# Performance work log

Measured on AMD Instinct MI355X. Metric: run time of the kernel, lower is better.

## Reference

```python
import jax, jax.numpy as jnp
import numpy as np

EPS = 1e-12  # torch F.normalize eps

def _l2norm(x, axis):
    n = jnp.sqrt(jnp.sum(x * x, axis=axis, keepdims=True))
    return x / jnp.maximum(n, EPS)

def setup_inputs() -> dict:
    key = jax.random.key(0)
    k1, k2, k3, k4 = jax.random.split(key, 4)
    B, Lq, Ld, D, NWAY = 128, 32, 180, 128, 8
    query_reps = jax.random.normal(k1, (B, Lq, D), dtype=jnp.float32)
    doc_reps = jax.random.normal(k2, (B, NWAY, Ld, D), dtype=jnp.float32)
    doc_mask = jax.random.randint(k3, (B, NWAY, Ld), 0, 2, dtype=jnp.int32)
    # labels are teacher log-probabilities (KLDivLoss log_target=True)
    labels = jax.nn.log_softmax(jax.random.normal(k4, (B, NWAY), dtype=jnp.float32), axis=-1)
    return {"query_reps": query_reps, "doc_reps": doc_reps, "doc_mask": doc_mask, "labels": labels}

def reference(query_reps, doc_reps, doc_mask, labels):
    # query: L2-normalize over feature dim (dim=2 in torch call)
    q = _l2norm(query_reps, axis=-1)                      # [B, Lq, D]
    # docs: mask padding tokens, then F.normalize with DEFAULT dim=1,
    # i.e. L2-normalize along the token axis (faithful to source).
    d = doc_reps * doc_mask[..., None].astype(doc_reps.dtype)  # [B, W, Ld, D]
    d = _l2norm(d, axis=2)
    # MaxSim: sim[b,w,q,l] = <q_bq, d_bwl>; max over doc tokens, sum over query tokens
    sim = jnp.einsum('bqd,bwld->bwql', q, d)              # [B, W, Lq, Ld]
    scores = jnp.max(sim, axis=-1).sum(axis=-1)           # [B, W]
    log_p = jax.nn.log_softmax(scores, axis=-1)           # == log(softmax(scores))
    # KLDivLoss(log_target=True, reduction='batchmean'): sum(exp(t)*(t - x)) / B
    B = scores.shape[0]
    loss = jnp.sum(jnp.exp(labels) * (labels - log_p)) / B
    return loss  # torch.mean of a scalar is the scalar
```

## Files before the change

kernel.cpp:

```cpp
#include <hip/hip_runtime.h>
#include <math.h>
#include <stdint.h>

#define NB 128
#define LQ 32
#define LD 180
#define DD 128
#define NW 8
#define NBW (NB*NW)
#define PB 40
#define LROWS 192

typedef __attribute__((ext_vector_type(8)))  short short8v;
typedef __attribute__((ext_vector_type(16))) float f32x16;

static __device__ __forceinline__ short bf16_rne(float f) {
    uint32_t u = __float_as_uint(f);
    uint32_t r = (u + 0x7fffu + ((u >> 16) & 1u)) >> 16;
    return (short)r;
}
static __device__ __forceinline__ float bf16_f32(short h) {
    return __uint_as_float(((uint32_t)(uint16_t)h) << 16);
}

__global__ __launch_bounds__(256) void qnorm_kernel(
    const float* __restrict__ qreps, float* __restrict__ qinv)
{
    const int t = threadIdx.x, b = blockIdx.x;
    const int r = t >> 3, sub = t & 7;
    const float4* qr = (const float4*)(qreps + (size_t)b * LQ * DD + r * DD + sub * 16);
    float ss = 0.f;
    #pragma unroll
    for (int k = 0; k < 4; ++k) {
        float4 v = qr[k];
        ss += v.x * v.x + v.y * v.y + v.z * v.z + v.w * v.w;
    }
    ss += __shfl_xor(ss, 4);
    ss += __shfl_xor(ss, 2);
    ss += __shfl_xor(ss, 1);
    if (sub == 0) qinv[b * LQ + r] = 1.0f / fmaxf(sqrtf(ss), 1e-12f);
}

__global__ __launch_bounds__(256, 4) void maxsim_kernel(
    const float* __restrict__ qreps, const float* __restrict__ dreps,
    const int* __restrict__ dmask, const float* __restrict__ qinv,
    float* __restrict__ scores)
{
    __shared__ short s_dh[LROWS * PB];
    __shared__ short s_dl[LROWS * PB];
    __shared__ short s_qh[LQ * PB];
    __shared__ short s_ql[LQ * PB];
    __shared__ float s_ssq[32 * 32];
    __shared__ float s_dinv[32];
    __shared__ float s_pm[4][LQ];

    const int t = threadIdx.x, bw = blockIdx.x, b = bw >> 3;
    const int lane = t & 63, wave = t >> 6;
    const int d4 = t & 7;
    const int rbase = t >> 3;
    const int lh = lane >> 5;
    const int l31 = lane & 31;

    const float4* doc4  = (const float4*)(dreps + (size_t)bw * LD * DD);
    const float4* q4g   = (const float4*)(qreps + (size_t)b * LQ * DD);
    const float*  qinvb = qinv + b * LQ;
    const int*    mrow  = dmask + bw * LD;

    float mk[6];
    #pragma unroll
    for (int s = 0; s < 6; ++s) {
        int l = rbase + 32 * s;
        mk[s] = (l < LD) ? (float)mrow[l] : 0.0f;
    }

    f32x16 acc0 = {};
    f32x16 acc1 = {};

    for (int cc = 0; cc < 4; ++cc) {
        if (cc) __syncthreads();

        float4 qv = q4g[rbase * 32 + cc * 8 + d4];

        float4 pssq = make_float4(0.f, 0.f, 0.f, 0.f);
        #pragma unroll
        for (int s = 0; s < 6; ++s) {
            int l = rbase + 32 * s;
            if (l < LD) {
                float4 v = doc4[l * 32 + cc * 8 + d4];
                float m = mk[s];
                v.x *= m; v.y *= m; v.z *= m; v.w *= m;
                pssq.x += v.x * v.x; pssq.y += v.y * v.y;
                pssq.z += v.z * v.z; pssq.w += v.w * v.w;
                short4 h, lo;
                h.x = bf16_rne(v.x); h.y = bf16_rne(v.y);
                h.z = bf16_rne(v.z); h.w = bf16_rne(v.w);
                lo.x = bf16_rne(v.x - bf16_f32(h.x));
                lo.y = bf16_rne(v.y - bf16_f32(h.y));
                lo.z = bf16_rne(v.z - bf16_f32(h.z));
                lo.w = bf16_rne(v.w - bf16_f32(h.w));
                *(short4*)&s_dh[l * PB + 4 * d4] = h;
                *(short4*)&s_dl[l * PB + 4 * d4] = lo;
            } else {
                short4 z = make_short4(0, 0, 0, 0);
                *(short4*)&s_dh[l * PB + 4 * d4] = z;
                *(short4*)&s_dl[l * PB + 4 * d4] = z;
            }
        }
        *(float4*)&s_ssq[rbase * 32 + 4 * d4] = pssq;
        __syncthreads();

        if (t < 32) {
            float tot = 0.f;
            #pragma unroll
            for (int g = 0; g < 32; ++g) tot += s_ssq[g * 32 + t];
            s_dinv[t] = 1.0f / fmaxf(sqrtf(tot), 1e-12f);
        }
        __syncthreads();

        {
            float qi = qinvb[rbase];
            float4 di = *(const float4*)&s_dinv[4 * d4];
            qv.x *= qi * di.x; qv.y *= qi * di.y;
            qv.z *= qi * di.z; qv.w *= qi * di.w;
            short4 h, lo;
            h.x = bf16_rne(qv.x); h.y = bf16_rne(qv.y);
            h.z = bf16_rne(qv.z); h.w = bf16_rne(qv.w);
            lo.x = bf16_rne(qv.x - bf16_f32(h.x));
            lo.y = bf16_rne(qv.y - bf16_f32(h.y));
            lo.z = bf16_rne(qv.z - bf16_f32(h.z));
            lo.w = bf16_rne(qv.w - bf16_f32(h.w));
            *(short4*)&s_qh[rbase * PB + 4 * d4] = h;
            *(short4*)&s_ql[rbase * PB + 4 * d4] = lo;
        }
        __syncthreads();

        #pragma unroll
        for (int kk = 0; kk < 2; ++kk) {
            const int ao = l31 * PB + 16 * kk + 8 * lh;
            short8v ah = *(const short8v*)&s_qh[ao];
            short8v al = *(const short8v*)&s_ql[ao];
            const int bo0 = (32 * wave + l31) * PB + 16 * kk + 8 * lh;
            short8v bh = *(const short8v*)&s_dh[bo0];
            short8v bl = *(const short8v*)&s_dl[bo0];
            acc0 = __builtin_amdgcn_mfma_f32_32x32x16_bf16(ah, bh, acc0, 0, 0, 0);
            acc0 = __builtin_amdgcn_mfma_f32_32x32x16_bf16(ah, bl, acc0, 0, 0, 0);
            acc0 = __builtin_amdgcn_mfma_f32_32x32x16_bf16(al, bh, acc0, 0, 0, 0);
            if (wave < 2) {
                const int bo1 = (32 * (wave + 4) + l31) * PB + 16 * kk + 8 * lh;
                short8v bh1 = *(const short8v*)&s_dh[bo1];
                short8v bl1 = *(const short8v*)&s_dl[bo1];
                acc1 = __builtin_amdgcn_mfma_f32_32x32x16_bf16(ah, bh1, acc1, 0, 0, 0);
                acc1 = __builtin_amdgcn_mfma_f32_32x32x16_bf16(ah, bl1, acc1, 0, 0, 0);
                acc1 = __builtin_amdgcn_mfma_f32_32x32x16_bf16(al, bh1, acc1, 0, 0, 0);
            }
        }
    }

    float pm[16];
    #pragma unroll
    for (int r = 0; r < 16; ++r) {
        float v = acc0[r];
        if (wave < 2) v = fmaxf(v, acc1[r]);
        pm[r] = v;
    }
    #pragma unroll
    for (int off = 1; off <= 16; off <<= 1)
        #pragma unroll
        for (int r = 0; r < 16; ++r)
            pm[r] = fmaxf(pm[r], __shfl_xor(pm[r], off));
    if (l31 == 0) {
        #pragma unroll
        for (int r = 0; r < 16; ++r)
            s_pm[wave][(r & 3) + 8 * (r >> 2) + 4 * lh] = pm[r];
    }
    __syncthreads();
    if (t < LQ) {
        float v = fmaxf(fmaxf(s_pm[0][t], s_pm[1][t]),
                        fmaxf(s_pm[2][t], s_pm[3][t]));
        #pragma unroll
        for (int off = 16; off >= 1; off >>= 1) v += __shfl_xor(v, off);
        if (t == 0) scores[bw] = v;
    }
}

__global__ __launch_bounds__(NB) void finish_kernel(
    const float* __restrict__ scores, const float* __restrict__ labels,
    float* __restrict__ out)
{
    __shared__ float s_part[2];
    const int t = threadIdx.x;
    const float* sr = scores + t * NW;
    const float* lr = labels + t * NW;

    float s[NW];
    float m = -INFINITY;
    #pragma unroll
    for (int w = 0; w < NW; ++w) { s[w] = sr[w]; m = fmaxf(m, s[w]); }
    float se = 0.f;
    #pragma unroll
    for (int w = 0; w < NW; ++w) se += expf(s[w] - m);
    float lse = logf(se) + m;

    float term = 0.f;
    #pragma unroll
    for (int w = 0; w < NW; ++w) {
        float lw = lr[w];
        term += expf(lw) * (lw - (s[w] - lse));
    }
    #pragma unroll
    for (int off = 32; off > 0; off >>= 1) term += __shfl_xor(term, off);
    if ((t & 63) == 0) s_part[t >> 6] = term;
    __syncthreads();
    if (t == 0) out[0] = (s_part[0] + s_part[1]) / (float)NB;
}

extern "C" void kernel_launch(void* const* d_in, const int* in_sizes, int n_in,
                              void* d_out, int out_size, void* d_ws, size_t ws_size,
                              hipStream_t stream) {
    const float* qreps  = (const float*)d_in[0];
    const float* dreps  = (const float*)d_in[1];
    const int*   dmask  = (const int*)d_in[2];
    const float* labels = (const float*)d_in[3];
    float* out = (float*)d_out;

    float* scores = (float*)d_ws;
    float* qinv   = scores + NBW;

    qnorm_kernel<<<NB, 256, 0, stream>>>(qreps, qinv);
    maxsim_kernel<<<NBW, 256, 0, stream>>>(qreps, dreps, dmask, qinv, scores);
    finish_kernel<<<1, NB, 0, stream>>>(scores, labels, out);
}
```

Before: 156.9 us.

## Fuse query norm into maxsim, use 512 threads, prefetch next doc chunk

Removes the separate query-normalisation kernel by computing query inverse norms inside each maxsim block. Blocks grow to 512 threads, so six waves each own one 32-row doc tile instead of four waves with two of them doing double work. The next K-chunk of doc and query data is register-prefetched while the current chunk is converted. Also cheaper bf16 splitting (truncation instead of RNE), a shuffle-based partial sum-of-squares reduction, and lighter barriers. The cost is redundant query-norm work per block, higher register pressure, and two idle waves during the MFMA phase.

```diff
diff --git a/kernel.cpp b/kernel.cpp
--- a/kernel.cpp
+++ b/kernel.cpp
@@ -14,169 +14,183 @@
 typedef __attribute__((ext_vector_type(8)))  short short8v;
 typedef __attribute__((ext_vector_type(16))) float f32x16;
 
-static __device__ __forceinline__ short bf16_rne(float f) {
-    uint32_t u = __float_as_uint(f);
-    uint32_t r = (u + 0x7fffu + ((u >> 16) & 1u)) >> 16;
-    return (short)r;
-}
-static __device__ __forceinline__ float bf16_f32(short h) {
-    return __uint_as_float(((uint32_t)(uint16_t)h) << 16);
-}
-
-__global__ __launch_bounds__(256) void qnorm_kernel(
-    const float* __restrict__ qreps, float* __restrict__ qinv)
-{
-    const int t = threadIdx.x, b = blockIdx.x;
-    const int r = t >> 3, sub = t & 7;
-    const float4* qr = (const float4*)(qreps + (size_t)b * LQ * DD + r * DD + sub * 16);
-    float ss = 0.f;
-    #pragma unroll
-    for (int k = 0; k < 4; ++k) {
-        float4 v = qr[k];
-        ss += v.x * v.x + v.y * v.y + v.z * v.z + v.w * v.w;
-    }
-    ss += __shfl_xor(ss, 4);
-    ss += __shfl_xor(ss, 2);
-    ss += __shfl_xor(ss, 1);
-    if (sub == 0) qinv[b * LQ + r] = 1.0f / fmaxf(sqrtf(ss), 1e-12f);
-}
-
-__global__ __launch_bounds__(256, 4) void maxsim_kernel(
+static __device__ __forceinline__ void bar() {
+    asm volatile("s_waitcnt lgkmcnt(0)" ::: "memory");
+    __builtin_amdgcn_s_barrier();
+}
+
+static __device__ __forceinline__ void split2(float x, short& h, short& l) {
+    uint32_t u = __float_as_uint(x);
+    h = (short)(u >> 16);
+    float r = x - __uint_as_float(u & 0xffff0000u);
+    l = (short)(__float_as_uint(r) >> 16);
+}
+
+__global__ __launch_bounds__(512, 4) void maxsim_kernel(
     const float* __restrict__ qreps, const float* __restrict__ dreps,
-    const int* __restrict__ dmask, const float* __restrict__ qinv,
-    float* __restrict__ scores)
+    const int* __restrict__ dmask, float* __restrict__ scores)
 {
     __shared__ short s_dh[LROWS * PB];
     __shared__ short s_dl[LROWS * PB];
     __shared__ short s_qh[LQ * PB];
     __shared__ short s_ql[LQ * PB];
-    __shared__ float s_ssq[32 * 32];
+    __shared__ float s_ssq[8 * 32];
     __shared__ float s_dinv[32];
-    __shared__ float s_pm[4][LQ];
+    __shared__ float s_qinv[32];
+    __shared__ float s_pm[6][LQ];
 
     const int t = threadIdx.x, bw = blockIdx.x, b = bw >> 3;
     const int lane = t & 63, wave = t >> 6;
     const int d4 = t & 7;
-    const int rbase = t >> 3;
-    const int lh = lane >> 5;
-    const int l31 = lane & 31;
-
-    const float4* doc4  = (const float4*)(dreps + (size_t)bw * LD * DD);
-    const float4* q4g   = (const float4*)(qreps + (size_t)b * LQ * DD);
-    const float*  qinvb = qinv + b * LQ;
-    const int*    mrow  = dmask + bw * LD;
-
-    float mk[6];
-    #pragma unroll
-    for (int s = 0; s < 6; ++s) {
-        int l = rbase + 32 * s;
-        mk[s] = (l < LD) ? (float)mrow[l] : 0.0f;
-    }
-
-    f32x16 acc0 = {};
-    f32x16 acc1 = {};
-
+    const int rb = t >> 3;
+    const int lh = lane >> 5, l31 = lane & 31;
+
+    const float4* doc4 = (const float4*)(dreps + (size_t)bw * LD * DD);
+    const float4* q4g  = (const float4*)(qreps + (size_t)b * LQ * DD);
+    const int*    mrow = dmask + bw * LD;
+
+    float4 dv0 = doc4[(rb      ) * 32 + d4];
+    float4 dv1 = doc4[(rb + 64 ) * 32 + d4];
+    float4 dv2;
+    if (rb < 52) dv2 = doc4[(rb + 128) * 32 + d4];
+    float4 qv, qn;
+    if (t < 256) qv = q4g[(t >> 3) * 32 + d4];
+
+    const float mk0 = (float)mrow[rb];
+    const float mk1 = (float)mrow[rb + 64];
+    const float mk2 = (rb < 52) ? (float)mrow[rb + 128] : 0.0f;
+
+    {
+        int r = t >> 4, sub = t & 15;
+        float4 a = q4g[r * 32 + sub];
+        float4 c = q4g[r * 32 + 16 + sub];
+        float ss = a.x*a.x + a.y*a.y + a.z*a.z + a.w*a.w
+                 + c.x*c.x + c.y*c.y + c.z*c.z + c.w*c.w;
+        ss += __shfl_xor(ss, 8);
+        ss += __shfl_xor(ss, 4);
+        ss += __shfl_xor(ss, 2);
+        ss += __shfl_xor(ss, 1);
+        if (sub == 0) s_qinv[r] = 1.0f / fmaxf(sqrtf(ss), 1e-12f);
+    }
+
+    f32x16 acc = {};
+
+    #pragma unroll
     for (int cc = 0; cc < 4; ++cc) {
-        if (cc) __syncthreads();
-
-        float4 qv = q4g[rbase * 32 + cc * 8 + d4];
+        if (cc) bar();
 
         float4 pssq = make_float4(0.f, 0.f, 0.f, 0.f);
-        #pragma unroll
-        for (int s = 0; s < 6; ++s) {
-            int l = rbase + 32 * s;
-            if (l < LD) {
-                float4 v = doc4[l * 32 + cc * 8 + d4];
-                float m = mk[s];
-                v.x *= m; v.y *= m; v.z *= m; v.w *= m;
-                pssq.x += v.x * v.x; pssq.y += v.y * v.y;
-                pssq.z += v.z * v.z; pssq.w += v.w * v.w;
-                short4 h, lo;
-                h.x = bf16_rne(v.x); h.y = bf16_rne(v.y);
-                h.z = bf16_rne(v.z); h.w = bf16_rne(v.w);
-                lo.x = bf16_rne(v.x - bf16_f32(h.x));
-                lo.y = bf16_rne(v.y - bf16_f32(h.y));
-                lo.z = bf16_rne(v.z - bf16_f32(h.z));
-                lo.w = bf16_rne(v.w - bf16_f32(h.w));
-                *(short4*)&s_dh[l * PB + 4 * d4] = h;
-                *(short4*)&s_dl[l * PB + 4 * d4] = lo;
-            } else {
-                short4 z = make_short4(0, 0, 0, 0);
-                *(short4*)&s_dh[l * PB + 4 * d4] = z;
-                *(short4*)&s_dl[l * PB + 4 * d4] = z;
-            }
-        }
-        *(float4*)&s_ssq[rbase * 32 + 4 * d4] = pssq;
-        __syncthreads();
+        {
+            float4 v = dv0; float m = mk0;
+            v.x *= m; v.y *= m; v.z *= m; v.w *= m;
+            pssq.x += v.x*v.x; pssq.y += v.y*v.y; pssq.z += v.z*v.z; pssq.w += v.w*v.w;
+            short4 h, lo;
+            split2(v.x, h.x, lo.x); split2(v.y, h.y, lo.y);
+            split2(v.z, h.z, lo.z); split2(v.w, h.w, lo.w);
+            *(short4*)&s_dh[rb * PB + 4 * d4] = h;
+            *(short4*)&s_dl[rb * PB + 4 * d4] = lo;
+        }
+        {
+            float4 v = dv1; float m = mk1;
+            v.x *= m; v.y *= m; v.z *= m; v.w *= m;
+            pssq.x += v.x*v.x; pssq.y += v.y*v.y; pssq.z += v.z*v.z; pssq.w += v.w*v.w;
+            short4 h, lo;
+            split2(v.x, h.x, lo.x); split2(v.y, h.y, lo.y);
+            split2(v.z, h.z, lo.z); split2(v.w, h.w, lo.w);
+            *(short4*)&s_dh[(rb + 64) * PB + 4 * d4] = h;
+            *(short4*)&s_dl[(rb + 64) * PB + 4 * d4] = lo;
+        }
+        if (rb < 52) {
+            float4 v = dv2; float m = mk2;
+            v.x *= m; v.y *= m; v.z *= m; v.w *= m;
+            pssq.x += v.x*v.x; pssq.y += v.y*v.y; pssq.z += v.z*v.z; pssq.w += v.w*v.w;
+            short4 h, lo;
+            split2(v.x, h.x, lo.x); split2(v.y, h.y, lo.y);
+            split2(v.z, h.z, lo.z); split2(v.w, h.w, lo.w);
+            *(short4*)&s_dh[(rb + 128) * PB + 4 * d4] = h;
+            *(short4*)&s_dl[(rb + 128) * PB + 4 * d4] = lo;
+        } else if (cc == 0) {
+            short4 z = make_short4(0, 0, 0, 0);
+            *(short4*)&s_dh[(rb + 128) * PB + 4 * d4] = z;
+            *(short4*)&s_dl[(rb + 128) * PB + 4 * d4] = z;
+        }
+
+        if (cc < 3) {
+            dv0 = doc4[(rb      ) * 32 + (cc + 1) * 8 + d4];
+            dv1 = doc4[(rb + 64 ) * 32 + (cc + 1) * 8 + d4];
+            if (rb < 52) dv2 = doc4[(rb + 128) * 32 + (cc + 1) * 8 + d4];
+            if (t < 256) qn = q4g[(t >> 3) * 32 + (cc + 1) * 8 + d4];
+        }
+
+        #pragma unroll
+        for (int off = 8; off <= 32; off <<= 1) {
+            pssq.x += __shfl_xor(pssq.x, off);
+            pssq.y += __shfl_xor(pssq.y, off);
+            pssq.z += __shfl_xor(pssq.z, off);
+            pssq.w += __shfl_xor(pssq.w, off);
+        }
+        if (lane < 8) *(float4*)&s_ssq[wave * 32 + 4 * lane] = pssq;
+        bar();
 
         if (t < 32) {
             float tot = 0.f;
             #pragma unroll
-            for (int g = 0; g < 32; ++g) tot += s_ssq[g * 32 + t];
+            for (int w = 0; w < 8; ++w) tot += s_ssq[w * 32 + t];
             s_dinv[t] = 1.0f / fmaxf(sqrtf(tot), 1e-12f);
         }
-        __syncthreads();
-
-        {
-            float qi = qinvb[rbase];
+        bar();
+
+        if (t < 256) {
+            float qi = s_qinv[t >> 3];
             float4 di = *(const float4*)&s_dinv[4 * d4];
-            qv.x *= qi * di.x; qv.y *= qi * di.y;
-            qv.z *= qi * di.z; qv.w *= qi * di.w;
-            short4 h, lo;
-            h.x = bf16_rne(qv.x); h.y = bf16_rne(qv.y);
-            h.z = bf16_rne(qv.z); h.w = bf16_rne(qv.w);
-            lo.x = bf16_rne(qv.x - bf16_f32(h.x));
-            lo.y = bf16_rne(qv.y - bf16_f32(h.y));
-            lo.z = bf16_rne(qv.z - bf16_f32(h.z));
-            lo.w = bf16_rne(qv.w - bf16_f32(h.w));
-            *(short4*)&s_qh[rbase * PB + 4 * d4] = h;
-            *(short4*)&s_ql[rbase * PB + 4 * d4] = lo;
-        }
-        __syncthreads();
-
-        #pragma unroll
-        for (int kk = 0; kk < 2; ++kk) {
-            const int ao = l31 * PB + 16 * kk + 8 * lh;
-            short8v ah = *(const short8v*)&s_qh[ao];
-            short8v al = *(const short8v*)&s_ql[ao];
-            const int bo0 = (32 * wave + l31) * PB + 16 * kk + 8 * lh;
-            short8v bh = *(const short8v*)&s_dh[bo0];
-            short8v bl = *(const short8v*)&s_dl[bo0];
-            acc0 = __builtin_amdgcn_mfma_f32_32x32x16_bf16(ah, bh, acc0, 0, 0, 0);
-            acc0 = __builtin_amdgcn_mfma_f32_32x32x16_bf16(ah, bl, acc0, 0, 0, 0);
-            acc0 = __builtin_amdgcn_mfma_f32_32x32x16_bf16(al, bh, acc0, 0, 0, 0);
-            if (wave < 2) {
-                const int bo1 = (32 * (wave + 4) + l31) * PB + 16 * kk + 8 * lh;
-                short8v bh1 = *(const short8v*)&s_dh[bo1];
-                short8v bl1 = *(const short8v*)&s_dl[bo1];
-                acc1 = __builtin_amdgcn_mfma_f32_32x32x16_bf16(ah, bh1, acc1, 0, 0, 0);
-                acc1 = __builtin_amdgcn_mfma_f32_32x32x16_bf16(ah, bl1, acc1, 0, 0, 0);
-                acc1 = __builtin_amdgcn_mfma_f32_32x32x16_bf16(al, bh1, acc1, 0, 0, 0);
+            float4 v = qv;
+            v.x *= qi * di.x; v.y *= qi * di.y;
+            v.z *= qi * di.z; v.w *= qi * di.w;
+            short4 h, lo;
+            split2(v.x, h.x, lo.x); split2(v.y, h.y, lo.y);
+            split2(v.z, h.z, lo.z); split2(v.w, h.w, lo.w);
+            *(short4*)&s_qh[(t >> 3) * PB + 4 * d4] = h;
+            *(short4*)&s_ql[(t >> 3) * PB + 4 * d4] = lo;
+        }
+        if (cc < 3) qv = qn;
+        bar();
+
+        if (wave < 6) {
+            #pragma unroll
+            for (int kk = 0; kk < 2; ++kk) {
+                int ao = l31 * PB + 16 * kk + 8 * lh;
+                short8v ah = *(const short8v*)&s_qh[ao];
+                short8v al = *(const short8v*)&s_ql[ao];
+                int bo = (32 * wave + l31) * PB + 16 * kk + 8 * lh;
+                short8v bh = *(const short8v*)&s_dh[bo];
+                short8v bl = *(const short8v*)&s_dl[bo];
+                acc = __builtin_amdgcn_mfma_f32_32x32x16_bf16(ah, bh, acc, 0, 0, 0);
+                acc = __builtin_amdgcn_mfma_f32_32x32x16_bf16(ah, bl, acc, 0, 0, 0);
+                acc = __builtin_amdgcn_mfma_f32_32x32x16_bf16(al, bh, acc, 0, 0, 0);
             }
         }
     }
 
-    float pm[16];
-    #pragma unroll
-    for (int r = 0; r < 16; ++r) {
-        float v = acc0[r];
-        if (wave < 2) v = fmaxf(v, acc1[r]);
-        pm[r] = v;
-    }
-    #pragma unroll
-    for (int off = 1; off <= 16; off <<= 1)
-        #pragma unroll
-        for (int r = 0; r < 16; ++r)
-            pm[r] = fmaxf(pm[r], __shfl_xor(pm[r], off));
-    if (l31 == 0) {
-        #pragma unroll
-        for (int r = 0; r < 16; ++r)
-            s_pm[wave][(r & 3) + 8 * (r >> 2) + 4 * lh] = pm[r];
-    }
-    __syncthreads();
-    if (t < LQ) {
-        float v = fmaxf(fmaxf(s_pm[0][t], s_pm[1][t]),
-                        fmaxf(s_pm[2][t], s_pm[3][t]));
+    if (wave < 6) {
+        float pm[16];
+        #pragma unroll
+        for (int r = 0; r < 16; ++r) pm[r] = acc[r];
+        #pragma unroll
+        for (int off = 1; off <= 16; off <<= 1)
+            #pragma unroll
+            for (int r = 0; r < 16; ++r)
+                pm[r] = fmaxf(pm[r], __shfl_xor(pm[r], off));
+        if (l31 == 0) {
+            #pragma unroll
+            for (int r = 0; r < 16; ++r)
+                s_pm[wave][(r & 3) + 8 * (r >> 2) + 4 * lh] = pm[r];
+        }
+    }
+    bar();
+    if (t < 32) {
+        float v = s_pm[0][t];
+        #pragma unroll
+        for (int w = 1; w < 6; ++w) v = fmaxf(v, s_pm[w][t]);
         #pragma unroll
         for (int off = 16; off >= 1; off >>= 1) v += __shfl_xor(v, off);
         if (t == 0) scores[bw] = v;
@@ -222,11 +236,8 @@
     const int*   dmask  = (const int*)d_in[2];
     const float* labels = (const float*)d_in[3];
     float* out = (float*)d_out;
-
     float* scores = (float*)d_ws;
-    float* qinv   = scores + NBW;
-
-    qnorm_kernel<<<NB, 256, 0, stream>>>(qreps, qinv);
-    maxsim_kernel<<<NBW, 256, 0, stream>>>(qreps, dreps, dmask, qinv, scores);
+
+    maxsim_kernel<<<NBW, 512, 0, stream>>>(qreps, dreps, dmask, scores);
     finish_kernel<<<1, NB, 0, stream>>>(scores, labels, out);
 }
```

After: 151.6 us. 3.4% less time.
